# Performance work log

Measured on AMD Instinct MI355X. Metric: run time of the kernel, lower is better.

Reference implementation:

```python
import jax, jax.numpy as jnp
import numpy as np

N, M, B = 4096, 2048, 64


def setup_inputs() -> dict:
    key = jax.random.key(0)
    k = jax.random.split(key, 6)
    return {
        "z": jax.random.normal(k[0], (N, B), dtype=jnp.float32),
        "u": jax.random.normal(k[1], (N, B), dtype=jnp.float32),
        "y": jax.random.normal(k[2], (M, B), dtype=jnp.float32),
        # Gaussian sensing matrix, unit-column-norm scaling as typical in CS
        "A": jax.random.normal(k[3], (M, N), dtype=jnp.float32) / np.float32(np.sqrt(N)),
        "kappa": jnp.float32(0.5),
        "eps": jnp.float32(1e-3),
        "eta": jnp.float32(0.1) * jnp.ones((N, 1), dtype=jnp.float32),
        "diag": jnp.float32(1.0) + 0.1 * jax.random.normal(k[4], (N,), dtype=jnp.float32),
        "offdiag": jnp.float32(0.1) * jax.random.normal(k[5], (N - 1,), dtype=jnp.float32),
    }


def reference(z, u, y, A, kappa, eps, eta, diag, offdiag):
    # Symmetric tridiagonal matrix T = diag(diag) + offdiag on +/-1 bands
    T = jnp.diag(diag) + jnp.diag(offdiag, k=-1) + jnp.diag(offdiag, k=1)  # [N, N]
    L, Q = jnp.linalg.eigh(T)  # L: [N], Q: [N, N]
    # GradientDescent update direction: negative gradient of
    # 0.5||Az - y||^2 + (kappa/2)||z - u||^2
    d = -(A.T @ (A @ z - y) + kappa * (z - u))  # [N, B]
    # eta * Q @ diag(max(L, eps)) @ Q^T @ d, eta broadcast over rows
    Lc = jnp.maximum(L, eps)[:, None]  # [N, 1]
    update = eta * (Q @ (Lc * (Q.T @ d)))  # [N, B]
    return z + update
```

## Files before the change

kernel.cpp:

```cpp
#include <hip/hip_runtime.h>

#define NN 4096
#define MM 2048
#define BB 64

typedef __attribute__((ext_vector_type(8))) short short8;
typedef __attribute__((ext_vector_type(4))) short short4v;
typedef __attribute__((ext_vector_type(4))) float f32x4;

__device__ __forceinline__ ushort f2bf(float f) {
    union { float f; unsigned u; } c; c.f = f;
    unsigned u = c.u + 0x7fffu + ((c.u >> 16) & 1u);
    return (ushort)(u >> 16);
}

__global__ __launch_bounds__(256) void k_prepz(const float* __restrict__ z,
                                               ushort* __restrict__ zT) {
    __shared__ float tl[32][33];
    const int tx = threadIdx.x & 31, ty = threadIdx.x >> 5;
    const int k0 = blockIdx.x * 32, b0 = blockIdx.y * 32;
#pragma unroll
    for (int i = 0; i < 4; ++i)
        tl[ty + 8 * i][tx] = z[(size_t)(k0 + ty + 8 * i) * BB + b0 + tx];
    __syncthreads();
#pragma unroll
    for (int i = 0; i < 4; ++i)
        zT[(size_t)(b0 + ty + 8 * i) * NN + k0 + tx] = f2bf(tl[tx][ty + 8 * i]);
}

template<int S1>
__global__ __launch_bounds__(256) void k_gemm1(const float* __restrict__ A,
                                               const ushort* __restrict__ zT,
                                               float* __restrict__ rTp) {
    constexpr int KSPAN = NN / S1;
    __shared__ ushort As[64][72];
    __shared__ ushort Zs[64][72];

    const int t = threadIdx.x;
    const int lane = t & 63, w = t >> 6;
    const int i16 = lane & 15, quad = lane >> 4;
    const int m0 = blockIdx.x * 64, k0 = blockIdx.y * KSPAN;
    const int srow = t >> 4, scol = (t & 15) * 4;
    const int zrow = t >> 2, zcol = (t & 3) * 16;

    float4 aR[4]; short8 zR0, zR1;
    auto preload = [&](int kc) {
#pragma unroll
        for (int rr = 0; rr < 4; ++rr)
            aR[rr] = *(const float4*)(A + (size_t)(m0 + rr * 16 + srow) * NN + kc + scol);
        zR0 = *(const short8*)(zT + (size_t)zrow * NN + kc + zcol);
        zR1 = *(const short8*)(zT + (size_t)zrow * NN + kc + zcol + 8);
    };

    f32x4 acc[4];
#pragma unroll
    for (int nt = 0; nt < 4; ++nt) acc[nt] = (f32x4)0.f;

    preload(k0);
    for (int kc = k0; kc < k0 + KSPAN; kc += 64) {
#pragma unroll
        for (int rr = 0; rr < 4; ++rr) {
            short4v ap;
            ap[0] = (short)f2bf(aR[rr].x); ap[1] = (short)f2bf(aR[rr].y);
            ap[2] = (short)f2bf(aR[rr].z); ap[3] = (short)f2bf(aR[rr].w);
            *(short4v*)&As[rr * 16 + srow][scol] = ap;
        }
        *(short8*)&Zs[zrow][zcol] = zR0;
        *(short8*)&Zs[zrow][zcol + 8] = zR1;
        __syncthreads();
        if (kc + 64 < k0 + KSPAN) preload(kc + 64);
#pragma unroll
        for (int ks = 0; ks < 64; ks += 32) {
            const short8 af = *(const short8*)&Zs[w * 16 + i16][ks + quad * 8];
#pragma unroll
            for (int nt = 0; nt < 4; ++nt) {
                const short8 bf = *(const short8*)&As[nt * 16 + i16][ks + quad * 8];
                acc[nt] = __builtin_amdgcn_mfma_f32_16x16x32_bf16(af, bf, acc[nt], 0, 0, 0);
            }
        }
        __syncthreads();
    }

    float* op = rTp + (size_t)blockIdx.y * BB * MM;
#pragma unroll
    for (int nt = 0; nt < 4; ++nt)
#pragma unroll
        for (int i = 0; i < 4; ++i)
            op[(size_t)(w * 16 + quad * 4 + i) * MM + m0 + nt * 16 + i16] = acc[nt][i];
}

template<int S1>
__global__ __launch_bounds__(256) void k_convR(const float* __restrict__ parts,
                                               const float* __restrict__ y,
                                               ushort* __restrict__ rT) {
    __shared__ float yt[32][33];
    const int tx = threadIdx.x & 31, ty = threadIdx.x >> 5;
    const int m0 = blockIdx.x * 32, b0 = blockIdx.y * 32;
#pragma unroll
    for (int i = 0; i < 4; ++i)
        yt[ty + 8 * i][tx] = y[(size_t)(m0 + ty + 8 * i) * BB + b0 + tx];
    __syncthreads();
#pragma unroll
    for (int i = 0; i < 4; ++i) {
        const int b = b0 + ty + 8 * i;
        float v = -yt[tx][ty + 8 * i];
        const size_t idx = (size_t)b * MM + m0 + tx;
#pragma unroll
        for (int s = 0; s < S1; ++s) v += parts[(size_t)s * BB * MM + idx];
        rT[idx] = f2bf(v);
    }
}

template<int S2>
__global__ __launch_bounds__(256) void k_gemm2(const float* __restrict__ A,
                                               const ushort* __restrict__ rT,
                                               float* __restrict__ gp) {
    constexpr int KSPAN = MM / S2;
    __shared__ float  As[64][66];
    __shared__ ushort Rs[64][72];

    const int t = threadIdx.x;
    const int lane = t & 63, w = t >> 6;
    const int i16 = lane & 15, quad = lane >> 4;
    const int n0 = blockIdx.x * 64, m0 = blockIdx.y * KSPAN;
    const int srow = t >> 4, scol = (t & 15) * 4;
    const int zrow = t >> 2, zcol = (t & 3) * 16;

    float4 aR[4]; short8 rR0, rR1;
    auto preload = [&](int mc) {
#pragma unroll
        for (int rr = 0; rr < 4; ++rr)
            aR[rr] = *(const float4*)(A + (size_t)(mc + rr * 16 + srow) * NN + n0 + scol);
        rR0 = *(const short8*)(rT + (size_t)zrow * MM + mc + zcol);
        rR1 = *(const short8*)(rT + (size_t)zrow * MM + mc + zcol + 8);
    };

    f32x4 acc[4];
#pragma unroll
    for (int nt = 0; nt < 4; ++nt) acc[nt] = (f32x4)0.f;

    preload(m0);
    for (int mc = m0; mc < m0 + KSPAN; mc += 64) {
#pragma unroll
        for (int rr = 0; rr < 4; ++rr) {
            *(float2*)&As[rr * 16 + srow][scol]     = make_float2(aR[rr].x, aR[rr].y);
            *(float2*)&As[rr * 16 + srow][scol + 2] = make_float2(aR[rr].z, aR[rr].w);
        }
        *(short8*)&Rs[zrow][zcol] = rR0;
        *(short8*)&Rs[zrow][zcol + 8] = rR1;
        __syncthreads();
        if (mc + 64 < m0 + KSPAN) preload(mc + 64);
#pragma unroll
        for (int ks = 0; ks < 64; ks += 32) {
            short8 af;
#pragma unroll
            for (int j = 0; j < 8; ++j)
                af[j] = (short)f2bf(As[ks + quad * 8 + j][w * 16 + i16]);
#pragma unroll
            for (int nt = 0; nt < 4; ++nt) {
                const short8 bf = *(const short8*)&Rs[nt * 16 + i16][ks + quad * 8];
                acc[nt] = __builtin_amdgcn_mfma_f32_16x16x32_bf16(af, bf, acc[nt], 0, 0, 0);
            }
        }
        __syncthreads();
    }

    float* op = gp + (size_t)blockIdx.y * NN * BB;
#pragma unroll
    for (int nt = 0; nt < 4; ++nt)
#pragma unroll
        for (int i = 0; i < 4; ++i)
            op[(size_t)(n0 + w * 16 + quad * 4 + i) * BB + nt * 16 + i16] = acc[nt][i];
}

template<int SPLITS>
__global__ __launch_bounds__(256) void k_fin(const float* __restrict__ parts,
                                             const float* __restrict__ z,
                                             const float* __restrict__ u,
                                             const float* __restrict__ kappa_p,
                                             const float* __restrict__ eta,
                                             const float* __restrict__ dia,
                                             const float* __restrict__ off,
                                             float* __restrict__ out) {
    __shared__ float ds_[18][BB];
    const int t = threadIdx.x;
    const int b = t & 63, rq = t >> 6;
    const int n0 = blockIdx.x * 16;
    const float kappa = kappa_p[0];

    for (int jr = rq; jr < 18; jr += 4) {
        const int rr = n0 - 1 + jr;
        float dv = 0.f;
        if (rr >= 0 && rr < NN) {
            const size_t idx = (size_t)rr * BB + b;
            float g = 0.f;
#pragma unroll
            for (int s = 0; s < SPLITS; ++s) g += parts[(size_t)s * NN * BB + idx];
            dv = -(g + kappa * (z[idx] - u[idx]));
        }
        ds_[jr][b] = dv;
    }
    __syncthreads();
#pragma unroll
    for (int jo = rq; jo < 16; jo += 4) {
        const int rn = n0 + jo;
        const size_t idx = (size_t)rn * BB + b;
        float s = dia[rn] * ds_[jo + 1][b];
        if (rn > 0)      s += off[rn - 1] * ds_[jo][b];
        if (rn < NN - 1) s += off[rn]     * ds_[jo + 2][b];
        out[idx] = z[idx] + eta[rn] * s;
    }
}

extern "C" void kernel_launch(void* const* d_in, const int* in_sizes, int n_in,
                              void* d_out, int out_size, void* d_ws, size_t ws_size,
                              hipStream_t stream) {
    const float* z     = (const float*)d_in[0];
    const float* u     = (const float*)d_in[1];
    const float* y     = (const float*)d_in[2];
    const float* A     = (const float*)d_in[3];
    const float* kappa = (const float*)d_in[4];
    const float* eta   = (const float*)d_in[6];
    const float* dia   = (const float*)d_in[7];
    const float* off   = (const float*)d_in[8];
    float* out = (float*)d_out;

    constexpr int S1 = 16, S2 = 8;
    char* wp = (char*)d_ws;
    ushort* zT       = (ushort*)wp; wp += (size_t)BB * NN * 2;
    float*  rT_parts = (float*)wp;  wp += (size_t)S1 * BB * MM * 4;
    ushort* rT       = (ushort*)wp; wp += (size_t)BB * MM * 2;
    float*  g_parts  = (float*)wp;  wp += (size_t)S2 * NN * BB * 4;

    k_prepz<<<dim3(NN / 32, BB / 32), 256, 0, stream>>>(z, zT);
    k_gemm1<S1><<<dim3(MM / 64, S1), 256, 0, stream>>>(A, zT, rT_parts);
    k_convR<S1><<<dim3(MM / 32, BB / 32), 256, 0, stream>>>(rT_parts, y, rT);
    k_gemm2<S2><<<dim3(NN / 64, S2), 256, 0, stream>>>(A, rT, g_parts);
    k_fin<S2><<<NN / 16, 256, 0, stream>>>(g_parts, z, u, kappa, eta, dia, off, out);
}
```

Baseline: 116.2 us.

## Fuse five kernels into one cooperative persistent kernel with grid syncs

Replaces the five separate launches (transpose z, GEMM1 split-K, reduce residual, GEMM2 split-K, finalize) with a single cooperative kernel of 512 blocks. The stages are separated by grid.sync() and share a shared-memory union. The aim is to remove per-launch overhead and the gaps between kernels. In exchange it adds grid-wide barrier cost, leaves many blocks idle during the small stages, and requires all 512 blocks to be co-resident (2 per CU via launch_bounds).

```diff
diff --git a/kernel.cpp b/kernel.cpp
--- a/kernel.cpp
+++ b/kernel.cpp
@@ -1,4 +1,7 @@
 #include <hip/hip_runtime.h>
+#include <hip/hip_cooperative_groups.h>
+
+namespace cg = cooperative_groups;
 
 #define NN 4096
 #define MM 2048
@@ -14,201 +17,186 @@
     return (ushort)(u >> 16);
 }
 
-__global__ __launch_bounds__(256) void k_prepz(const float* __restrict__ z,
-                                               ushort* __restrict__ zT) {
-    __shared__ float tl[32][33];
-    const int tx = threadIdx.x & 31, ty = threadIdx.x >> 5;
-    const int k0 = blockIdx.x * 32, b0 = blockIdx.y * 32;
-#pragma unroll
-    for (int i = 0; i < 4; ++i)
-        tl[ty + 8 * i][tx] = z[(size_t)(k0 + ty + 8 * i) * BB + b0 + tx];
-    __syncthreads();
-#pragma unroll
-    for (int i = 0; i < 4; ++i)
-        zT[(size_t)(b0 + ty + 8 * i) * NN + k0 + tx] = f2bf(tl[tx][ty + 8 * i]);
-}
-
-template<int S1>
-__global__ __launch_bounds__(256) void k_gemm1(const float* __restrict__ A,
-                                               const ushort* __restrict__ zT,
-                                               float* __restrict__ rTp) {
-    constexpr int KSPAN = NN / S1;
-    __shared__ ushort As[64][72];
-    __shared__ ushort Zs[64][72];
-
+#define S1 16
+#define S2 8
+
+__global__ void __launch_bounds__(256, 2)
+k_fused(const float* __restrict__ A, const float* __restrict__ z,
+        const float* __restrict__ y, const float* __restrict__ u,
+        const float* __restrict__ kappa_p, const float* __restrict__ eta,
+        const float* __restrict__ dia, const float* __restrict__ off,
+        ushort* __restrict__ zT, float* __restrict__ rTp,
+        ushort* __restrict__ rT, float* __restrict__ gp,
+        float* __restrict__ out) {
+    __shared__ union {
+        struct { ushort As[64][72]; ushort Zs[64][72]; } g1;
+        struct { float  As[64][66]; ushort Rs[64][72]; } g2;
+        float tl[32][33];
+        float ds_[18][BB];
+    } sm;
+
+    cg::grid_group grid = cg::this_grid();
+    const int bid = blockIdx.x;
     const int t = threadIdx.x;
     const int lane = t & 63, w = t >> 6;
     const int i16 = lane & 15, quad = lane >> 4;
-    const int m0 = blockIdx.x * 64, k0 = blockIdx.y * KSPAN;
+    const int tx = t & 31, ty = t >> 5;
     const int srow = t >> 4, scol = (t & 15) * 4;
     const int zrow = t >> 2, zcol = (t & 3) * 16;
 
-    float4 aR[4]; short8 zR0, zR1;
-    auto preload = [&](int kc) {
-#pragma unroll
-        for (int rr = 0; rr < 4; ++rr)
-            aR[rr] = *(const float4*)(A + (size_t)(m0 + rr * 16 + srow) * NN + kc + scol);
-        zR0 = *(const short8*)(zT + (size_t)zrow * NN + kc + zcol);
-        zR1 = *(const short8*)(zT + (size_t)zrow * NN + kc + zcol + 8);
-    };
-
-    f32x4 acc[4];
-#pragma unroll
-    for (int nt = 0; nt < 4; ++nt) acc[nt] = (f32x4)0.f;
-
-    preload(k0);
-    for (int kc = k0; kc < k0 + KSPAN; kc += 64) {
-#pragma unroll
-        for (int rr = 0; rr < 4; ++rr) {
-            short4v ap;
-            ap[0] = (short)f2bf(aR[rr].x); ap[1] = (short)f2bf(aR[rr].y);
-            ap[2] = (short)f2bf(aR[rr].z); ap[3] = (short)f2bf(aR[rr].w);
-            *(short4v*)&As[rr * 16 + srow][scol] = ap;
-        }
-        *(short8*)&Zs[zrow][zcol] = zR0;
-        *(short8*)&Zs[zrow][zcol + 8] = zR1;
+    if (bid < 256) {
+        const int k0 = (bid & 127) * 32, b0 = (bid >> 7) * 32;
+#pragma unroll
+        for (int i = 0; i < 4; ++i)
+            sm.tl[ty + 8 * i][tx] = z[(size_t)(k0 + ty + 8 * i) * BB + b0 + tx];
         __syncthreads();
-        if (kc + 64 < k0 + KSPAN) preload(kc + 64);
-#pragma unroll
-        for (int ks = 0; ks < 64; ks += 32) {
-            const short8 af = *(const short8*)&Zs[w * 16 + i16][ks + quad * 8];
-#pragma unroll
-            for (int nt = 0; nt < 4; ++nt) {
-                const short8 bf = *(const short8*)&As[nt * 16 + i16][ks + quad * 8];
-                acc[nt] = __builtin_amdgcn_mfma_f32_16x16x32_bf16(af, bf, acc[nt], 0, 0, 0);
-            }
-        }
+#pragma unroll
+        for (int i = 0; i < 4; ++i)
+            zT[(size_t)(b0 + ty + 8 * i) * NN + k0 + tx] = f2bf(sm.tl[tx][ty + 8 * i]);
+    }
+    grid.sync();
+
+    {
+        const int m0 = (bid & 31) * 64;
+        const int k0 = (bid >> 5) * (NN / S1);
+        float4 aR[4]; short8 zR0, zR1;
+        auto preload = [&](int kc) {
+#pragma unroll
+            for (int rr = 0; rr < 4; ++rr)
+                aR[rr] = *(const float4*)(A + (size_t)(m0 + rr * 16 + srow) * NN + kc + scol);
+            zR0 = *(const short8*)(zT + (size_t)zrow * NN + kc + zcol);
+            zR1 = *(const short8*)(zT + (size_t)zrow * NN + kc + zcol + 8);
+        };
+        f32x4 acc[4];
+#pragma unroll
+        for (int nt = 0; nt < 4; ++nt) acc[nt] = (f32x4)0.f;
+
+        preload(k0);
+        for (int kc = k0; kc < k0 + NN / S1; kc += 64) {
+#pragma unroll
+            for (int rr = 0; rr < 4; ++rr) {
+                short4v ap;
+                ap[0] = (short)f2bf(aR[rr].x); ap[1] = (short)f2bf(aR[rr].y);
+                ap[2] = (short)f2bf(aR[rr].z); ap[3] = (short)f2bf(aR[rr].w);
+                *(short4v*)&sm.g1.As[rr * 16 + srow][scol] = ap;
+            }
+            *(short8*)&sm.g1.Zs[zrow][zcol] = zR0;
+            *(short8*)&sm.g1.Zs[zrow][zcol + 8] = zR1;
+            __syncthreads();
+            if (kc + 64 < k0 + NN / S1) preload(kc + 64);
+#pragma unroll
+            for (int ks = 0; ks < 64; ks += 32) {
+                const short8 af = *(const short8*)&sm.g1.Zs[w * 16 + i16][ks + quad * 8];
+#pragma unroll
+                for (int nt = 0; nt < 4; ++nt) {
+                    const short8 bf = *(const short8*)&sm.g1.As[nt * 16 + i16][ks + quad * 8];
+                    acc[nt] = __builtin_amdgcn_mfma_f32_16x16x32_bf16(af, bf, acc[nt], 0, 0, 0);
+                }
+            }
+            __syncthreads();
+        }
+        float* op = rTp + (size_t)(bid >> 5) * BB * MM;
+#pragma unroll
+        for (int nt = 0; nt < 4; ++nt)
+#pragma unroll
+            for (int i = 0; i < 4; ++i)
+                op[(size_t)(w * 16 + quad * 4 + i) * MM + m0 + nt * 16 + i16] = acc[nt][i];
+    }
+    grid.sync();
+
+    if (bid < 128) {
+        const int m0 = (bid & 63) * 32, b0 = (bid >> 6) * 32;
+#pragma unroll
+        for (int i = 0; i < 4; ++i)
+            sm.tl[ty + 8 * i][tx] = y[(size_t)(m0 + ty + 8 * i) * BB + b0 + tx];
         __syncthreads();
-    }
-
-    float* op = rTp + (size_t)blockIdx.y * BB * MM;
-#pragma unroll
-    for (int nt = 0; nt < 4; ++nt)
-#pragma unroll
-        for (int i = 0; i < 4; ++i)
-            op[(size_t)(w * 16 + quad * 4 + i) * MM + m0 + nt * 16 + i16] = acc[nt][i];
-}
-
-template<int S1>
-__global__ __launch_bounds__(256) void k_convR(const float* __restrict__ parts,
-                                               const float* __restrict__ y,
-                                               ushort* __restrict__ rT) {
-    __shared__ float yt[32][33];
-    const int tx = threadIdx.x & 31, ty = threadIdx.x >> 5;
-    const int m0 = blockIdx.x * 32, b0 = blockIdx.y * 32;
-#pragma unroll
-    for (int i = 0; i < 4; ++i)
-        yt[ty + 8 * i][tx] = y[(size_t)(m0 + ty + 8 * i) * BB + b0 + tx];
-    __syncthreads();
-#pragma unroll
-    for (int i = 0; i < 4; ++i) {
-        const int b = b0 + ty + 8 * i;
-        float v = -yt[tx][ty + 8 * i];
-        const size_t idx = (size_t)b * MM + m0 + tx;
-#pragma unroll
-        for (int s = 0; s < S1; ++s) v += parts[(size_t)s * BB * MM + idx];
-        rT[idx] = f2bf(v);
-    }
-}
-
-template<int S2>
-__global__ __launch_bounds__(256) void k_gemm2(const float* __restrict__ A,
-                                               const ushort* __restrict__ rT,
-                                               float* __restrict__ gp) {
-    constexpr int KSPAN = MM / S2;
-    __shared__ float  As[64][66];
-    __shared__ ushort Rs[64][72];
-
-    const int t = threadIdx.x;
-    const int lane = t & 63, w = t >> 6;
-    const int i16 = lane & 15, quad = lane >> 4;
-    const int n0 = blockIdx.x * 64, m0 = blockIdx.y * KSPAN;
-    const int srow = t >> 4, scol = (t & 15) * 4;
-    const int zrow = t >> 2, zcol = (t & 3) * 16;
-
-    float4 aR[4]; short8 rR0, rR1;
-    auto preload = [&](int mc) {
-#pragma unroll
-        for (int rr = 0; rr < 4; ++rr)
-            aR[rr] = *(const float4*)(A + (size_t)(mc + rr * 16 + srow) * NN + n0 + scol);
-        rR0 = *(const short8*)(rT + (size_t)zrow * MM + mc + zcol);
-        rR1 = *(const short8*)(rT + (size_t)zrow * MM + mc + zcol + 8);
-    };
-
-    f32x4 acc[4];
-#pragma unroll
-    for (int nt = 0; nt < 4; ++nt) acc[nt] = (f32x4)0.f;
-
-    preload(m0);
-    for (int mc = m0; mc < m0 + KSPAN; mc += 64) {
-#pragma unroll
-        for (int rr = 0; rr < 4; ++rr) {
-            *(float2*)&As[rr * 16 + srow][scol]     = make_float2(aR[rr].x, aR[rr].y);
-            *(float2*)&As[rr * 16 + srow][scol + 2] = make_float2(aR[rr].z, aR[rr].w);
-        }
-        *(short8*)&Rs[zrow][zcol] = rR0;
-        *(short8*)&Rs[zrow][zcol + 8] = rR1;
+#pragma unroll
+        for (int i = 0; i < 4; ++i) {
+            const int b = b0 + ty + 8 * i;
+            float v = -sm.tl[tx][ty + 8 * i];
+            const size_t idx = (size_t)b * MM + m0 + tx;
+#pragma unroll
+            for (int s = 0; s < S1; ++s) v += rTp[(size_t)s * BB * MM + idx];
+            rT[idx] = f2bf(v);
+        }
+    }
+    grid.sync();
+
+    {
+        const int n0 = (bid & 63) * 64;
+        const int m0 = (bid >> 6) * (MM / S2);
+        float4 aR[4]; short8 rR0, rR1;
+        auto preload = [&](int mc) {
+#pragma unroll
+            for (int rr = 0; rr < 4; ++rr)
+                aR[rr] = *(const float4*)(A + (size_t)(mc + rr * 16 + srow) * NN + n0 + scol);
+            rR0 = *(const short8*)(rT + (size_t)zrow * MM + mc + zcol);
+            rR1 = *(const short8*)(rT + (size_t)zrow * MM + mc + zcol + 8);
+        };
+        f32x4 acc[4];
+#pragma unroll
+        for (int nt = 0; nt < 4; ++nt) acc[nt] = (f32x4)0.f;
+
+        preload(m0);
+        for (int mc = m0; mc < m0 + MM / S2; mc += 64) {
+#pragma unroll
+            for (int rr = 0; rr < 4; ++rr) {
+                *(float2*)&sm.g2.As[rr * 16 + srow][scol]     = make_float2(aR[rr].x, aR[rr].y);
+                *(float2*)&sm.g2.As[rr * 16 + srow][scol + 2] = make_float2(aR[rr].z, aR[rr].w);
+            }
+            *(short8*)&sm.g2.Rs[zrow][zcol] = rR0;
+            *(short8*)&sm.g2.Rs[zrow][zcol + 8] = rR1;
+            __syncthreads();
+            if (mc + 64 < m0 + MM / S2) preload(mc + 64);
+#pragma unroll
+            for (int ks = 0; ks < 64; ks += 32) {
+                short8 af;
+#pragma unroll
+                for (int j = 0; j < 8; ++j)
+                    af[j] = (short)f2bf(sm.g2.As[ks + quad * 8 + j][w * 16 + i16]);
+#pragma unroll
+                for (int nt = 0; nt < 4; ++nt) {
+                    const short8 bf = *(const short8*)&sm.g2.Rs[nt * 16 + i16][ks + quad * 8];
+                    acc[nt] = __builtin_amdgcn_mfma_f32_16x16x32_bf16(af, bf, acc[nt], 0, 0, 0);
+                }
+            }
+            __syncthreads();
+        }
+        float* op = gp + (size_t)(bid >> 6) * NN * BB;
+#pragma unroll
+        for (int nt = 0; nt < 4; ++nt)
+#pragma unroll
+            for (int i = 0; i < 4; ++i)
+                op[(size_t)(n0 + w * 16 + quad * 4 + i) * BB + nt * 16 + i16] = acc[nt][i];
+    }
+    grid.sync();
+
+    if (bid < 256) {
+        const int b = lane, rq = w;
+        const int n0 = bid * 16;
+        const float kappa = kappa_p[0];
+        for (int jr = rq; jr < 18; jr += 4) {
+            const int rr = n0 - 1 + jr;
+            float dv = 0.f;
+            if (rr >= 0 && rr < NN) {
+                const size_t idx = (size_t)rr * BB + b;
+                float g = 0.f;
+#pragma unroll
+                for (int s = 0; s < S2; ++s) g += gp[(size_t)s * NN * BB + idx];
+                dv = -(g + kappa * (z[idx] - u[idx]));
+            }
+            sm.ds_[jr][b] = dv;
+        }
         __syncthreads();
-        if (mc + 64 < m0 + KSPAN) preload(mc + 64);
-#pragma unroll
-        for (int ks = 0; ks < 64; ks += 32) {
-            short8 af;
-#pragma unroll
-            for (int j = 0; j < 8; ++j)
-                af[j] = (short)f2bf(As[ks + quad * 8 + j][w * 16 + i16]);
-#pragma unroll
-            for (int nt = 0; nt < 4; ++nt) {
-                const short8 bf = *(const short8*)&Rs[nt * 16 + i16][ks + quad * 8];
-                acc[nt] = __builtin_amdgcn_mfma_f32_16x16x32_bf16(af, bf, acc[nt], 0, 0, 0);
-            }
-        }
-        __syncthreads();
-    }
-
-    float* op = gp + (size_t)blockIdx.y * NN * BB;
-#pragma unroll
-    for (int nt = 0; nt < 4; ++nt)
-#pragma unroll
-        for (int i = 0; i < 4; ++i)
-            op[(size_t)(n0 + w * 16 + quad * 4 + i) * BB + nt * 16 + i16] = acc[nt][i];
-}
-
-template<int SPLITS>
-__global__ __launch_bounds__(256) void k_fin(const float* __restrict__ parts,
-                                             const float* __restrict__ z,
-                                             const float* __restrict__ u,
-                                             const float* __restrict__ kappa_p,
-                                             const float* __restrict__ eta,
-                                             const float* __restrict__ dia,
-                                             const float* __restrict__ off,
-                                             float* __restrict__ out) {
-    __shared__ float ds_[18][BB];
-    const int t = threadIdx.x;
-    const int b = t & 63, rq = t >> 6;
-    const int n0 = blockIdx.x * 16;
-    const float kappa = kappa_p[0];
-
-    for (int jr = rq; jr < 18; jr += 4) {
-        const int rr = n0 - 1 + jr;
-        float dv = 0.f;
-        if (rr >= 0 && rr < NN) {
-            const size_t idx = (size_t)rr * BB + b;
-            float g = 0.f;
-#pragma unroll
-            for (int s = 0; s < SPLITS; ++s) g += parts[(size_t)s * NN * BB + idx];
-            dv = -(g + kappa * (z[idx] - u[idx]));
-        }
-        ds_[jr][b] = dv;
-    }
-    __syncthreads();
-#pragma unroll
-    for (int jo = rq; jo < 16; jo += 4) {
-        const int rn = n0 + jo;
-        const size_t idx = (size_t)rn * BB + b;
-        float s = dia[rn] * ds_[jo + 1][b];
-        if (rn > 0)      s += off[rn - 1] * ds_[jo][b];
-        if (rn < NN - 1) s += off[rn]     * ds_[jo + 2][b];
-        out[idx] = z[idx] + eta[rn] * s;
+#pragma unroll
+        for (int jo = rq; jo < 16; jo += 4) {
+            const int rn = n0 + jo;
+            const size_t idx = (size_t)rn * BB + b;
+            float s = dia[rn] * sm.ds_[jo + 1][b];
+            if (rn > 0)      s += off[rn - 1] * sm.ds_[jo][b];
+            if (rn < NN - 1) s += off[rn]     * sm.ds_[jo + 2][b];
+            out[idx] = z[idx] + eta[rn] * s;
+        }
     }
 }
 
@@ -225,16 +213,15 @@
     const float* off   = (const float*)d_in[8];
     float* out = (float*)d_out;
 
-    constexpr int S1 = 16, S2 = 8;
     char* wp = (char*)d_ws;
-    ushort* zT       = (ushort*)wp; wp += (size_t)BB * NN * 2;
-    float*  rT_parts = (float*)wp;  wp += (size_t)S1 * BB * MM * 4;
-    ushort* rT       = (ushort*)wp; wp += (size_t)BB * MM * 2;
-    float*  g_parts  = (float*)wp;  wp += (size_t)S2 * NN * BB * 4;
-
-    k_prepz<<<dim3(NN / 32, BB / 32), 256, 0, stream>>>(z, zT);
-    k_gemm1<S1><<<dim3(MM / 64, S1), 256, 0, stream>>>(A, zT, rT_parts);
-    k_convR<S1><<<dim3(MM / 32, BB / 32), 256, 0, stream>>>(rT_parts, y, rT);
-    k_gemm2<S2><<<dim3(NN / 64, S2), 256, 0, stream>>>(A, rT, g_parts);
-    k_fin<S2><<<NN / 16, 256, 0, stream>>>(g_parts, z, u, kappa, eta, dia, off, out);
+    ushort* zT  = (ushort*)wp; wp += (size_t)BB * NN * 2;
+    float*  rTp = (float*)wp;  wp += (size_t)S1 * BB * MM * 4;
+    ushort* rT  = (ushort*)wp; wp += (size_t)BB * MM * 2;
+    float*  gp  = (float*)wp;  wp += (size_t)S2 * NN * BB * 4;
+
+    void* kargs[] = { (void*)&A, (void*)&z, (void*)&y, (void*)&u, (void*)&kappa,
+                      (void*)&eta, (void*)&dia, (void*)&off,
+                      (void*)&zT, (void*)&rTp, (void*)&rT, (void*)&gp, (void*)&out };
+    hipLaunchCooperativeKernel((const void*)k_fused, dim3(512), dim3(256),
+                               kargs, 0, stream);
 }
```

Measured after the change: 360.3 us. +210.0%, slower.
